# Performance work log

Hardware: AMD Instinct MI355X
Metric: run time of the kernel (lower is better)

Reference implementation:

```python
import jax, jax.numpy as jnp
import numpy as np

NC = 64
B, H, W = 32, 128, 128


def setup_inputs() -> dict:
    key = jax.random.key(0)
    kx, = jax.random.split(key, 1)
    x = jax.random.normal(kx, (B, NC, H, W), dtype=jnp.float32)
    # params as initialized in the torch module
    exp_param = jnp.eye(NC, dtype=jnp.float32)[:, :, None, None]  # (nc, nc, 1, 1)
    bias = jnp.zeros((NC, 1, 1), dtype=jnp.float32)               # (nc, 1, 1)
    return {"x": x, "exp_param": exp_param, "bias": bias}


def reference(x, exp_param, bias):
    # x: (B, nc, H, W); exp_param: (nc, nc, 1, 1); bias: (nc, 1, 1)
    xr = jax.nn.relu(x) + 0.1  # strictly positive -> log is safe
    # prod_i xr[b,i,h,w] ** E[i,j]  ==  exp( sum_i E[i,j] * log xr[b,i,h,w] )
    # Fused form avoids materializing the (B, nc, nc, H, W) intermediate.
    E = exp_param[:, :, 0, 0]  # (nc_in=i, nc_out=j)
    logx = jnp.log(xr)
    out = jnp.exp(jnp.einsum('bihw,ij->bjhw', logx, E)) + bias  # (B, nc, H, W)
    return out
```

## Files before the change

kernel.cpp:

```cpp
#include <hip/hip_runtime.h>

#define NCH 64
#define HWSZ 16384
#define NPOINTS (32 * HWSZ)

__global__ __launch_bounds__(256, 2) void fused_log_einsum_exp(
    const float* __restrict__ x,
    const float* __restrict__ E,
    const float* __restrict__ bias,
    float* __restrict__ out)
{
    const int p  = blockIdx.x * 256 + threadIdx.x;
    const int b  = p >> 14;
    const int hw = p & (HWSZ - 1);

    const float* xp = x   + (size_t)b * NCH * HWSZ + hw;
    float*       op = out + (size_t)b * NCH * HWSZ + hw;

    float acc[NCH];
    #pragma unroll
    for (int j = 0; j < NCH; ++j) acc[j] = 0.0f;

    #pragma unroll 4
    for (int i = 0; i < NCH; ++i) {
        float v  = xp[(size_t)i * HWSZ];
        float lx = __logf(fmaxf(v, 0.0f) + 0.1f);
        #pragma unroll
        for (int j = 0; j < NCH; ++j)
            acc[j] = fmaf(lx, E[i * NCH + j], acc[j]);
    }

    #pragma unroll
    for (int j = 0; j < NCH; ++j)
        op[(size_t)j * HWSZ] = __expf(acc[j]) + bias[j];
}

extern "C" void kernel_launch(void* const* d_in, const int* in_sizes, int n_in,
                              void* d_out, int out_size, void* d_ws, size_t ws_size,
                              hipStream_t stream) {
    const float* x    = (const float*)d_in[0];
    const float* E    = (const float*)d_in[1];
    const float* bias = (const float*)d_in[2];
    float* out = (float*)d_out;

    dim3 grid(NPOINTS / 256), block(256);
    hipLaunchKernelGGL(fused_log_einsum_exp, grid, block, 0, stream,
                       x, E, bias, out);
}
```

Before: 257.0 us.

## Stage log values in LDS and split output channels across warps

Each block now handles 64 spatial points. The log of the input is computed once per point and channel and staged in shared memory, and the four wavefronts each compute 16 of the 64 output channels. This cuts per-thread accumulators from 64 to 16, which lowers register pressure and lets more blocks fit per CU (launch bounds raised to 4). The cost is a syncthreads and LDS reads. Memory accesses also become narrower, at 64 contiguous floats per channel row.

```diff
diff --git a/kernel.cpp b/kernel.cpp
--- a/kernel.cpp
+++ b/kernel.cpp
@@ -3,36 +3,55 @@
 #define NCH 64
 #define HWSZ 16384
 #define NPOINTS (32 * HWSZ)
+#define TILE_P 64
+#define JPT 16
 
-__global__ __launch_bounds__(256, 2) void fused_log_einsum_exp(
+__global__ __launch_bounds__(256, 4) void fused_log_einsum_exp(
     const float* __restrict__ x,
     const float* __restrict__ E,
     const float* __restrict__ bias,
     float* __restrict__ out)
 {
-    const int p  = blockIdx.x * 256 + threadIdx.x;
-    const int b  = p >> 14;
-    const int hw = p & (HWSZ - 1);
+    __shared__ float lxs[NCH][TILE_P];
 
-    const float* xp = x   + (size_t)b * NCH * HWSZ + hw;
-    float*       op = out + (size_t)b * NCH * HWSZ + hw;
+    const int t   = threadIdx.x;
+    const int p0  = blockIdx.x * TILE_P;
+    const int b   = p0 >> 14;
+    const int hw0 = p0 & (HWSZ - 1);
 
-    float acc[NCH];
+    const float* xb = x   + (size_t)b * NCH * HWSZ + hw0;
+    float*       ob = out + (size_t)b * NCH * HWSZ + hw0;
+
+    {
+        const int p  = t & 63;
+        const int i0 = (t >> 6) * 16;
+        #pragma unroll
+        for (int k = 0; k < 16; ++k) {
+            const int i = i0 + k;
+            float v = xb[(size_t)i * HWSZ + p];
+            lxs[i][p] = __logf(fmaxf(v, 0.0f) + 0.1f);
+        }
+    }
+    __syncthreads();
+
+    const int p  = t & 63;
+    const int j0 = __builtin_amdgcn_readfirstlane((t >> 6) * JPT);
+
+    float acc[JPT];
     #pragma unroll
-    for (int j = 0; j < NCH; ++j) acc[j] = 0.0f;
+    for (int k = 0; k < JPT; ++k) acc[k] = 0.0f;
 
     #pragma unroll 4
     for (int i = 0; i < NCH; ++i) {
-        float v  = xp[(size_t)i * HWSZ];
-        float lx = __logf(fmaxf(v, 0.0f) + 0.1f);
+        const float lx = lxs[i][p];
         #pragma unroll
-        for (int j = 0; j < NCH; ++j)
-            acc[j] = fmaf(lx, E[i * NCH + j], acc[j]);
+        for (int k = 0; k < JPT; ++k)
+            acc[k] = fmaf(lx, E[i * NCH + j0 + k], acc[k]);
     }
 
     #pragma unroll
-    for (int j = 0; j < NCH; ++j)
-        op[(size_t)j * HWSZ] = __expf(acc[j]) + bias[j];
+    for (int k = 0; k < JPT; ++k)
+        ob[(size_t)(j0 + k) * HWSZ + p] = __expf(acc[k]) + bias[j0 + k];
 }
 
 extern "C" void kernel_launch(void* const* d_in, const int* in_sizes, int n_in,
@@ -43,7 +62,7 @@
     const float* bias = (const float*)d_in[2];
     float* out = (float*)d_out;
 
-    dim3 grid(NPOINTS / 256), block(256);
+    dim3 grid(NPOINTS / TILE_P), block(256);
     hipLaunchKernelGGL(fused_log_einsum_exp, grid, block, 0, stream,
                        x, E, bias, out);
 }
```

Result: faster. 247.8 us (-3.6%).

## Compute channel mixing with split-bf16 MFMA and a persistent tile loop

Applied to the files above, without the earlier changes.

Replaces the per-thread scalar 64x64 FMA loop with MFMA 16x16x32 bf16 instructions. Both E and log(x) are split into high and low bf16 parts, and three MFMAs per k-chunk approximate fp32 accuracy. E fragments and bias are loaded into registers once per block, and a fixed grid of 1024 blocks strides over 64-point tiles. This removes the heavy FP32 ALU work and the register pressure of the 64-entry accumulator array. In exchange it adds split-precision error, and global loads and stores become 16-lane-coalesced segments per channel row.

```diff
diff --git a/kernel.cpp b/kernel.cpp
--- a/kernel.cpp
+++ b/kernel.cpp
@@ -3,6 +3,18 @@
 #define NCH 64
 #define HWSZ 16384
 #define NPOINTS (32 * HWSZ)
+#define NTILES (NPOINTS / 64)
+#define NBLOCKS 1024
+
+typedef __attribute__((ext_vector_type(8))) short bf16x8;
+typedef __attribute__((ext_vector_type(4))) float f32x4;
+
+static __device__ __forceinline__ unsigned short bf16_trunc(float f) {
+    return (unsigned short)(__float_as_uint(f) >> 16);
+}
+static __device__ __forceinline__ float bf16_up(unsigned short h) {
+    return __uint_as_float((unsigned)h << 16);
+}
 
 __global__ __launch_bounds__(256, 2) void fused_log_einsum_exp(
     const float* __restrict__ x,
@@ -10,29 +22,79 @@
     const float* __restrict__ bias,
     float* __restrict__ out)
 {
-    const int p  = blockIdx.x * 256 + threadIdx.x;
-    const int b  = p >> 14;
-    const int hw = p & (HWSZ - 1);
+    const int lane = threadIdx.x & 63;
+    const int wv   = threadIdx.x >> 6;
+    const int lg   = lane >> 4;
+    const int ln   = lane & 15;
 
-    const float* xp = x   + (size_t)b * NCH * HWSZ + hw;
-    float*       op = out + (size_t)b * NCH * HWSZ + hw;
-
-    float acc[NCH];
+    bf16x8 ah[4][2], al[4][2];
     #pragma unroll
-    for (int j = 0; j < NCH; ++j) acc[j] = 0.0f;
-
-    #pragma unroll 4
-    for (int i = 0; i < NCH; ++i) {
-        float v  = xp[(size_t)i * HWSZ];
-        float lx = __logf(fmaxf(v, 0.0f) + 0.1f);
+    for (int m = 0; m < 4; ++m) {
         #pragma unroll
-        for (int j = 0; j < NCH; ++j)
-            acc[j] = fmaf(lx, E[i * NCH + j], acc[j]);
+        for (int kk = 0; kk < 2; ++kk) {
+            bf16x8 h, l;
+            #pragma unroll
+            for (int e = 0; e < 8; ++e) {
+                const int i = kk * 32 + lg * 8 + e;
+                const int j = m * 16 + ln;
+                const float v = E[i * NCH + j];
+                const unsigned short hh = bf16_trunc(v);
+                h[e] = (short)hh;
+                l[e] = (short)bf16_trunc(v - bf16_up(hh));
+            }
+            ah[m][kk] = h; al[m][kk] = l;
+        }
     }
 
+    float bv[4][4];
     #pragma unroll
-    for (int j = 0; j < NCH; ++j)
-        op[(size_t)j * HWSZ] = __expf(acc[j]) + bias[j];
+    for (int m = 0; m < 4; ++m)
+        #pragma unroll
+        for (int r = 0; r < 4; ++r)
+            bv[m][r] = bias[m * 16 + lg * 4 + r];
+
+    for (int t = blockIdx.x; t < NTILES; t += NBLOCKS) {
+        const int p0 = t * 64 + wv * 16;
+        const size_t base = (size_t)(p0 & ~(HWSZ - 1)) * NCH
+                          + (size_t)(p0 & (HWSZ - 1)) + ln;
+
+        float xr[2][8];
+        #pragma unroll
+        for (int kk = 0; kk < 2; ++kk)
+            #pragma unroll
+            for (int e = 0; e < 8; ++e)
+                xr[kk][e] = x[base + (size_t)(kk * 32 + lg * 8 + e) * HWSZ];
+
+        bf16x8 bh[2], bl[2];
+        #pragma unroll
+        for (int kk = 0; kk < 2; ++kk) {
+            bf16x8 h, l;
+            #pragma unroll
+            for (int e = 0; e < 8; ++e) {
+                const float lx = __logf(fmaxf(xr[kk][e], 0.0f) + 0.1f);
+                const unsigned short hh = bf16_trunc(lx);
+                h[e] = (short)hh;
+                l[e] = (short)bf16_trunc(lx - bf16_up(hh));
+            }
+            bh[kk] = h; bl[kk] = l;
+        }
+
+        #pragma unroll
+        for (int m = 0; m < 4; ++m) {
+            f32x4 acc = {0.f, 0.f, 0.f, 0.f};
+            #pragma unroll
+            for (int kk = 0; kk < 2; ++kk) {
+                acc = __builtin_amdgcn_mfma_f32_16x16x32_bf16(ah[m][kk], bh[kk], acc, 0, 0, 0);
+                acc = __builtin_amdgcn_mfma_f32_16x16x32_bf16(ah[m][kk], bl[kk], acc, 0, 0, 0);
+                acc = __builtin_amdgcn_mfma_f32_16x16x32_bf16(al[m][kk], bh[kk], acc, 0, 0, 0);
+            }
+            #pragma unroll
+            for (int r = 0; r < 4; ++r) {
+                const int j = m * 16 + lg * 4 + r;
+                out[base + (size_t)j * HWSZ] = __expf(acc[r]) + bv[m][r];
+            }
+        }
+    }
 }
 
 extern "C" void kernel_launch(void* const* d_in, const int* in_sizes, int n_in,
@@ -43,7 +105,7 @@
     const float* bias = (const float*)d_in[2];
     float* out = (float*)d_out;
 
-    dim3 grid(NPOINTS / 256), block(256);
+    dim3 grid(NBLOCKS), block(256);
     hipLaunchKernelGGL(fused_log_einsum_exp, grid, block, 0, stream,
                        x, E, bias, out);
 }
```

Result: faster. 244.4 us (-4.9%).

## Use bf16 MFMA with hi/lo split for channel mixing, persistent double-buffered tiles

Applied to the files above, without the earlier changes.

Replaces the per-thread scalar FMA loop over 64x64 channel weights with MFMA 16x16x32 bf16 instructions. The log activations are split into high and low bf16 parts to recover precision, while the weight matrix E is truncated to bf16. The kernel is also made persistent with 1024 blocks, each processing 8 tiles of 64 points with two register buffers so the next tile's loads overlap the current tile's compute. The aim is to remove the heavy ALU cost of 4096 FMAs per point and the register pressure of 64 accumulators. The risk is lost precision from truncating E to bf16, although it is exact for the identity initialisation.

```diff
diff --git a/kernel.cpp b/kernel.cpp
--- a/kernel.cpp
+++ b/kernel.cpp
@@ -3,6 +3,20 @@
 #define NCH 64
 #define HWSZ 16384
 #define NPOINTS (32 * HWSZ)
+#define NTILES (NPOINTS / 64)
+#define NBLOCKS 1024
+
+typedef __attribute__((ext_vector_type(8))) short bf16x8;
+typedef __attribute__((ext_vector_type(4))) float f32x4;
+
+union fragU { bf16x8 v; unsigned int u[4]; };
+
+static __device__ __forceinline__ unsigned int fbits(float f) {
+    return __float_as_uint(f);
+}
+static __device__ __forceinline__ float bf16_up_bits(unsigned int b) {
+    return __uint_as_float(b & 0xFFFF0000u);
+}
 
 __global__ __launch_bounds__(256, 2) void fused_log_einsum_exp(
     const float* __restrict__ x,
@@ -10,29 +24,98 @@
     const float* __restrict__ bias,
     float* __restrict__ out)
 {
-    const int p  = blockIdx.x * 256 + threadIdx.x;
-    const int b  = p >> 14;
-    const int hw = p & (HWSZ - 1);
+    const int lane = threadIdx.x & 63;
+    const int wv   = threadIdx.x >> 6;
+    const int lg   = lane >> 4;
+    const int ln   = lane & 15;
 
-    const float* xp = x   + (size_t)b * NCH * HWSZ + hw;
-    float*       op = out + (size_t)b * NCH * HWSZ + hw;
-
-    float acc[NCH];
+    bf16x8 ah[4][2];
     #pragma unroll
-    for (int j = 0; j < NCH; ++j) acc[j] = 0.0f;
-
-    #pragma unroll 4
-    for (int i = 0; i < NCH; ++i) {
-        float v  = xp[(size_t)i * HWSZ];
-        float lx = __logf(fmaxf(v, 0.0f) + 0.1f);
+    for (int m = 0; m < 4; ++m) {
         #pragma unroll
-        for (int j = 0; j < NCH; ++j)
-            acc[j] = fmaf(lx, E[i * NCH + j], acc[j]);
+        for (int kk = 0; kk < 2; ++kk) {
+            fragU h;
+            #pragma unroll
+            for (int w = 0; w < 4; ++w) {
+                const int i0 = kk * 32 + lg * 8 + 2 * w;
+                const int j  = m * 16 + ln;
+                h.u[w] = (fbits(E[(i0 + 1) * NCH + j]) & 0xFFFF0000u)
+                       | (fbits(E[i0 * NCH + j]) >> 16);
+            }
+            ah[m][kk] = h.v;
+        }
     }
 
+    float bv[4][4];
     #pragma unroll
-    for (int j = 0; j < NCH; ++j)
-        op[(size_t)j * HWSZ] = __expf(acc[j]) + bias[j];
+    for (int m = 0; m < 4; ++m)
+        #pragma unroll
+        for (int r = 0; r < 4; ++r)
+            bv[m][r] = bias[m * 16 + lg * 4 + r];
+
+    const int t0 = blockIdx.x;
+
+#define TILE_BASE(T) ((size_t)(((T) * 64 + wv * 16) & ~(HWSZ - 1)) * NCH \
+                    + (size_t)(((T) * 64 + wv * 16) & (HWSZ - 1)) + ln)
+
+#define LOAD_TILE(XR, BASE)                                                  \
+    { _Pragma("unroll")                                                      \
+      for (int e = 0; e < 16; ++e)                                           \
+          XR[e] = x[(BASE) + (size_t)((e >> 3) * 32 + lg * 8 + (e & 7)) * HWSZ]; }
+
+#define COMPUTE_TILE(XR, BASE)                                               \
+    { bf16x8 bh[2], bl[2];                                                   \
+      _Pragma("unroll")                                                      \
+      for (int kk = 0; kk < 2; ++kk) {                                       \
+          fragU h_, l_;                                                      \
+          _Pragma("unroll")                                                  \
+          for (int w = 0; w < 4; ++w) {                                      \
+              const float lx0 = __logf(fmaxf(XR[kk * 8 + 2 * w],     0.0f) + 0.1f); \
+              const float lx1 = __logf(fmaxf(XR[kk * 8 + 2 * w + 1], 0.0f) + 0.1f); \
+              h_.u[w] = (fbits(lx1) & 0xFFFF0000u) | (fbits(lx0) >> 16);     \
+              const float lo0 = lx0 - bf16_up_bits(fbits(lx0));              \
+              const float lo1 = lx1 - bf16_up_bits(fbits(lx1));              \
+              l_.u[w] = (fbits(lo1) & 0xFFFF0000u) | (fbits(lo0) >> 16);     \
+          }                                                                  \
+          bh[kk] = h_.v; bl[kk] = l_.v;                                      \
+      }                                                                      \
+      _Pragma("unroll")                                                      \
+      for (int m = 0; m < 4; ++m) {                                          \
+          f32x4 acc = {0.f, 0.f, 0.f, 0.f};                                  \
+          _Pragma("unroll")                                                  \
+          for (int kk = 0; kk < 2; ++kk) {                                   \
+              acc = __builtin_amdgcn_mfma_f32_16x16x32_bf16(ah[m][kk], bh[kk], acc, 0, 0, 0); \
+              acc = __builtin_amdgcn_mfma_f32_16x16x32_bf16(ah[m][kk], bl[kk], acc, 0, 0, 0); \
+          }                                                                  \
+          _Pragma("unroll")                                                  \
+          for (int r = 0; r < 4; ++r)                                        \
+              out[(BASE) + (size_t)(m * 16 + lg * 4 + r) * HWSZ] =           \
+                  __expf(acc[r]) + bv[m][r];                                 \
+      } }
+
+    float xA[16], xB[16];
+    size_t baseA = TILE_BASE(t0);
+    size_t baseB = TILE_BASE(t0 + NBLOCKS);
+    LOAD_TILE(xA, baseA);
+    LOAD_TILE(xB, baseB);
+
+    #pragma unroll
+    for (int k = 0; k < 4; ++k) {
+        COMPUTE_TILE(xA, baseA);
+        if (k < 3) {
+            baseA = TILE_BASE(t0 + (2 * k + 2) * NBLOCKS);
+            LOAD_TILE(xA, baseA);
+        }
+        COMPUTE_TILE(xB, baseB);
+        if (k < 3) {
+            baseB = TILE_BASE(t0 + (2 * k + 3) * NBLOCKS);
+            LOAD_TILE(xB, baseB);
+        }
+    }
+
+#undef TILE_BASE
+#undef LOAD_TILE
+#undef COMPUTE_TILE
 }
 
 extern "C" void kernel_launch(void* const* d_in, const int* in_sizes, int n_in,
@@ -43,7 +126,7 @@
     const float* bias = (const float*)d_in[2];
     float* out = (float*)d_out;
 
-    dim3 grid(NPOINTS / 256), block(256);
+    dim3 grid(NBLOCKS), block(256);
     hipLaunchKernelGGL(fused_log_einsum_exp, grid, block, 0, stream,
                        x, E, bias, out);
 }
```

After: 251.4 us. 2.2% less time.
